# Performance work log

Measured on AMD Instinct MI355X. Metric: run time of the kernel, lower is better.

Reference implementation:

```python
import jax, jax.numpy as jnp
import numpy as np

NEG_SLOPE = 0.2  # PyG GATConv default negative_slope
EPS = 1e-16      # PyG softmax denominator epsilon


def gat_conv(x, src, dst, W, b, att_src, att_dst, num_nodes):
    """PyG GATConv, heads=1, add_self_loops=True (self loops already in src/dst).
    x: [N, Fin]; src/dst: [E]; W: [Fin, Fout]; att_src/att_dst: [Fout]."""
    h = x @ W                                  # [N, Fout]
    a_src = h @ att_src                        # [N]
    a_dst = h @ att_dst                        # [N]
    e = jax.nn.leaky_relu(a_src[src] + a_dst[dst], NEG_SLOPE)  # [E]
    m = jax.ops.segment_max(e, dst, num_segments=num_nodes)    # softmax over edges grouped by dst
    ex = jnp.exp(e - m[dst])
    denom = jax.ops.segment_sum(ex, dst, num_segments=num_nodes)
    alpha = ex / (denom[dst] + EPS)            # [E]
    out = jax.ops.segment_sum(alpha[:, None] * h[src], dst, num_segments=num_nodes)
    return out + b


def global_attention(x, gate_w, gate_b):
    """PyG GlobalAttention with a single graph: softmax(gate_nn(x)) weighted sum."""
    gate = x @ gate_w + gate_b                 # [N, 1]
    attn = jax.nn.softmax(gate, axis=0)        # softmax over all nodes (one graph)
    return jnp.sum(attn * x, axis=0, keepdims=True)  # [1, F]


def setup_inputs() -> dict:
    key = jax.random.key(0)
    ks = jax.random.split(key, 12)
    N, E, D, H = 50000, 800000, 768, 256
    x = jax.random.normal(ks[0], (N, D), dtype=jnp.float32)
    edge_index = jax.random.randint(ks[1], (2, E), 0, N, dtype=jnp.int64)
    s = 1.0 / np.sqrt(D)
    W1 = jax.random.normal(ks[2], (D, H), dtype=jnp.float32) * s
    b1 = jnp.zeros((H,), dtype=jnp.float32)
    as1 = jax.random.normal(ks[3], (H,), dtype=jnp.float32) * (1.0 / np.sqrt(H))
    ad1 = jax.random.normal(ks[4], (H,), dtype=jnp.float32) * (1.0 / np.sqrt(H))
    s2 = 1.0 / np.sqrt(H)
    W2 = jax.random.normal(ks[5], (H, H), dtype=jnp.float32) * s2
    b2 = jnp.zeros((H,), dtype=jnp.float32)
    as2 = jax.random.normal(ks[6], (H,), dtype=jnp.float32) * s2
    ad2 = jax.random.normal(ks[7], (H,), dtype=jnp.float32) * s2
    gate_w = jax.random.normal(ks[8], (H, 1), dtype=jnp.float32) * s2
    gate_b = jnp.zeros((1,), dtype=jnp.float32)
    return {"x": x, "edge_index": edge_index, "W1": W1, "b1": b1, "as1": as1,
            "ad1": ad1, "W2": W2, "b2": b2, "as2": as2, "ad2": ad2,
            "gate_w": gate_w, "gate_b": gate_b}


def reference(x, edge_index, W1, b1, as1, ad1, W2, b2, as2, ad2, gate_w, gate_b):
    N = x.shape[0]
    loops = jnp.arange(N, dtype=edge_index.dtype)
    src = jnp.concatenate([edge_index[0], loops])  # add self loops (GATConv default)
    dst = jnp.concatenate([edge_index[1], loops])
    h = gat_conv(x, src, dst, W1, b1, as1, ad1, N)
    h = jax.nn.relu(h)
    h = gat_conv(h, src, dst, W2, b2, as2, ad2, N)
    h = jax.nn.relu(h)
    return global_attention(h, gate_w, gate_b)   # [1, 256]
```

## Files before the change

kernel.cpp:

```cpp
#include <hip/hip_runtime.h>

#define WAVE 64
#define LRELU(x) ((x) > 0.0f ? (x) : 0.2f * (x))
#define SB0 __builtin_amdgcn_sched_barrier(0)

typedef __attribute__((ext_vector_type(8))) short bf16x8;
typedef __attribute__((ext_vector_type(8))) unsigned short u16x8;
typedef __attribute__((ext_vector_type(4))) float f32x4;

__device__ __forceinline__ void gld16(const void* g, void* l) {
    __builtin_amdgcn_global_load_lds((const __attribute__((address_space(1))) unsigned int*)g,
                                     (__attribute__((address_space(3))) unsigned int*)l,
                                     16, 0, 0);
}

__device__ __forceinline__ unsigned short f2bf_hi(float f) {
    unsigned u = __builtin_bit_cast(unsigned, f);
    u += 0x7FFF + ((u >> 16) & 1);
    return (unsigned short)(u >> 16);
}

__device__ __forceinline__ void split8(f32x4 a, f32x4 b, bf16x8& hi, bf16x8& lo) {
    float f[8] = {a[0], a[1], a[2], a[3], b[0], b[1], b[2], b[3]};
#pragma unroll
    for (int e = 0; e < 8; e++) {
        unsigned u = __builtin_bit_cast(unsigned, f[e]);
        float hf = __builtin_bit_cast(float, u & 0xFFFF0000u);
        float fl = f[e] - hf;
        unsigned u2 = __builtin_bit_cast(unsigned, fl);
        unsigned t2 = u2 + 0x7FFF + ((u2 >> 16) & 1);
        hi[e] = (short)(u >> 16);
        lo[e] = (short)(t2 >> 16);
    }
}

__device__ __forceinline__ void split8t(f32x4 a, f32x4 b, bf16x8& hi, bf16x8& lo) {
    float f[8] = {a[0], a[1], a[2], a[3], b[0], b[1], b[2], b[3]};
#pragma unroll
    for (int e = 0; e < 8; e++) {
        unsigned u = __builtin_bit_cast(unsigned, f[e]);
        float hf = __builtin_bit_cast(float, u & 0xFFFF0000u);
        float fl = f[e] - hf;
        unsigned u2 = __builtin_bit_cast(unsigned, fl);
        hi[e] = (short)(u >> 16);
        lo[e] = (short)(u2 >> 16);
    }
}

__global__ __launch_bounds__(512) void k_gemm_f32A(const float* __restrict__ A,
                                                   const unsigned short* __restrict__ Bh,
                                                   unsigned short* __restrict__ Cb,
                                                   float* __restrict__ asrc,
                                                   float* __restrict__ adst,
                                                   const float* __restrict__ att_s,
                                                   const float* __restrict__ att_d,
                                                   int M, int K) {
    __shared__ char smem[49152];
    char* bA = smem;
    char* bB = smem + 32768;

    const int tid = threadIdx.x, lane = tid & 63, w = tid >> 6;
    const int m16 = lane & 15, q = lane >> 4;
    const int mq = w >> 1, nh = w & 1;
    const int row0 = blockIdx.x * 128, col0 = blockIdx.y * 128;
    const int NT = K >> 5;

    f32x4 acc[2][4];
#pragma unroll
    for (int i = 0; i < 2; i++)
#pragma unroll
        for (int j = 0; j < 4; j++) acc[i][j] = (f32x4){0.f, 0.f, 0.f, 0.f};

    const float* apt[2];
    const int jA0 = w * 2;
#pragma unroll
    for (int jj = 0; jj < 2; jj++) {
        int j = jA0 + jj;
        int r = j * 8 + (lane >> 3);
        int grow = row0 + r;
        if (grow > M - 1) grow = M - 1;
        int s = (lane & 7) ^ ((lane >> 3) & 7);
        apt[jj] = A + (size_t)grow * K + s * 4;
    }
    const unsigned short* bpt;
    {
        int r = w * 16 + (lane >> 2);
        int s = (lane & 3) ^ ((lane >> 3) & 3);
        bpt = Bh + (size_t)(col0 + r) * K + s * 8;
    }

    auto stage = [&](int t, int buf) {
        gld16(bpt + (size_t)t * 32, bB + buf * 8192 + w * 1024);
#pragma unroll
        for (int jj = 0; jj < 2; jj++)
            gld16(apt[jj] + (size_t)t * 32, bA + buf * 16384 + (jA0 + jj) * 1024);
    };

    stage(0, 0); SB0;
    asm volatile("s_waitcnt vmcnt(0)" ::: "memory");
    __builtin_amdgcn_s_barrier();

    for (int t = 0; t < NT; ++t) {
        if (t + 1 < NT) stage(t + 1, (t + 1) & 1);
        SB0;

        const char* A_ = bA + (t & 1) * 16384;
        const char* B_ = bB + (t & 1) * 8192;
        bf16x8 bh[4];
#pragma unroll
        for (int nt = 0; nt < 4; nt++) {
            int r = nh * 64 + nt * 16 + m16;
            int p = q ^ ((r >> 1) & 3);
            bh[nt] = *(const bf16x8*)(B_ + r * 64 + p * 16);
        }
#pragma unroll
        for (int mt = 0; mt < 2; mt++) {
            int r = mq * 32 + mt * 16 + m16;
            int p0 = (2 * q) ^ (r & 7);
            int p1 = (2 * q + 1) ^ (r & 7);
            f32x4 a0 = *(const f32x4*)(A_ + r * 128 + p0 * 16);
            f32x4 a1 = *(const f32x4*)(A_ + r * 128 + p1 * 16);
            bf16x8 ah, al;
            split8t(a0, a1, ah, al);
#pragma unroll
            for (int nt = 0; nt < 4; nt++) {
                acc[mt][nt] = __builtin_amdgcn_mfma_f32_16x16x32_bf16(ah, bh[nt], acc[mt][nt], 0, 0, 0);
                acc[mt][nt] = __builtin_amdgcn_mfma_f32_16x16x32_bf16(al, bh[nt], acc[mt][nt], 0, 0, 0);
            }
        }
        SB0;
        asm volatile("s_waitcnt vmcnt(0)" ::: "memory");
        __builtin_amdgcn_s_barrier();
    }

    const int rbase = row0 + mq * 32;
    const int cbase = col0 + nh * 64;
#pragma unroll
    for (int mt = 0; mt < 2; mt++)
#pragma unroll
        for (int r = 0; r < 4; r++) {
            int row = rbase + mt * 16 + q * 4 + r;
            if (row < M) {
#pragma unroll
                for (int nt = 0; nt < 4; nt++)
                    Cb[(size_t)row * 256 + cbase + nt * 16 + m16] = f2bf_hi(acc[mt][nt][r]);
            }
        }
    float as_v[4], ad_v[4];
#pragma unroll
    for (int nt = 0; nt < 4; nt++) {
        as_v[nt] = att_s[cbase + nt * 16 + m16];
        ad_v[nt] = att_d[cbase + nt * 16 + m16];
    }
#pragma unroll
    for (int mt = 0; mt < 2; mt++)
#pragma unroll
        for (int r = 0; r < 4; r++) {
            float s = 0.f, d = 0.f;
#pragma unroll
            for (int nt = 0; nt < 4; nt++) {
                float v = acc[mt][nt][r];
                s = fmaf(v, as_v[nt], s);
                d = fmaf(v, ad_v[nt], d);
            }
#pragma unroll
            for (int off = 1; off < 16; off <<= 1) {
                s += __shfl_xor(s, off);
                d += __shfl_xor(d, off);
            }
            int row = rbase + mt * 16 + q * 4 + r;
            if (m16 == 0 && row < M) {
                atomicAdd(&asrc[row], s);
                atomicAdd(&adst[row], d);
            }
        }
}

__global__ __launch_bounds__(512) void k_gemm_bf16A(const unsigned short* __restrict__ Ah,
                                                    const unsigned short* __restrict__ Al,
                                                    const unsigned short* __restrict__ Bh,
                                                    unsigned short* __restrict__ Cb,
                                                    float* __restrict__ asrc,
                                                    float* __restrict__ adst,
                                                    const float* __restrict__ att_s,
                                                    const float* __restrict__ att_d,
                                                    int M, int K) {
    __shared__ char smem[49152];
    char* bAh = smem;
    char* bAl = smem + 16384;
    char* bB  = smem + 32768;

    const int tid = threadIdx.x, lane = tid & 63, w = tid >> 6;
    const int m16 = lane & 15, q = lane >> 4;
    const int mq = w >> 1, nh = w & 1;
    const int row0 = blockIdx.x * 128, col0 = blockIdx.y * 128;
    const int NT = K >> 5;

    f32x4 acc[2][4];
#pragma unroll
    for (int i = 0; i < 2; i++)
#pragma unroll
        for (int j = 0; j < 4; j++) acc[i][j] = (f32x4){0.f, 0.f, 0.f, 0.f};

    const unsigned short* ahpt;
    const unsigned short* alpt;
    const unsigned short* bpt;
    {
        int r = w * 16 + (lane >> 2);
        int s = (lane & 3) ^ ((lane >> 3) & 3);
        ahpt = Ah + (size_t)(row0 + r) * K + s * 8;
        alpt = Al + (size_t)(row0 + r) * K + s * 8;
        bpt  = Bh + (size_t)(col0 + r) * K + s * 8;
    }

    auto stage = [&](int t, int buf) {
        gld16(bpt  + (size_t)t * 32, bB  + buf * 8192 + w * 1024);
        gld16(ahpt + (size_t)t * 32, bAh + buf * 8192 + w * 1024);
        gld16(alpt + (size_t)t * 32, bAl + buf * 8192 + w * 1024);
    };

    stage(0, 0); SB0;
    asm volatile("s_waitcnt vmcnt(0)" ::: "memory");
    __builtin_amdgcn_s_barrier();

    for (int t = 0; t < NT; ++t) {
        if (t + 1 < NT) stage(t + 1, (t + 1) & 1);
        SB0;

        const char* Ah_ = bAh + (t & 1) * 8192;
        const char* Al_ = bAl + (t & 1) * 8192;
        const char* B_  = bB  + (t & 1) * 8192;
        bf16x8 bh[4];
#pragma unroll
        for (int nt = 0; nt < 4; nt++) {
            int r = nh * 64 + nt * 16 + m16;
            int p = q ^ ((r >> 1) & 3);
            bh[nt] = *(const bf16x8*)(B_ + r * 64 + p * 16);
        }
#pragma unroll
        for (int mt = 0; mt < 2; mt++) {
            int r = mq * 32 + mt * 16 + m16;
            int p = q ^ ((r >> 1) & 3);
            bf16x8 ah = *(const bf16x8*)(Ah_ + r * 64 + p * 16);
            bf16x8 al = *(const bf16x8*)(Al_ + r * 64 + p * 16);
#pragma unroll
            for (int nt = 0; nt < 4; nt++) {
                acc[mt][nt] = __builtin_amdgcn_mfma_f32_16x16x32_bf16(ah, bh[nt], acc[mt][nt], 0, 0, 0);
                acc[mt][nt] = __builtin_amdgcn_mfma_f32_16x16x32_bf16(al, bh[nt], acc[mt][nt], 0, 0, 0);
            }
        }
        SB0;
        asm volatile("s_waitcnt vmcnt(0)" ::: "memory");
        __builtin_amdgcn_s_barrier();
    }

    const int rbase = row0 + mq * 32;
    const int cbase = col0 + nh * 64;
#pragma unroll
    for (int mt = 0; mt < 2; mt++)
#pragma unroll
        for (int r = 0; r < 4; r++) {
            int row = rbase + mt * 16 + q * 4 + r;
            if (row < M) {
#pragma unroll
                for (int nt = 0; nt < 4; nt++)
                    Cb[(size_t)row * 256 + cbase + nt * 16 + m16] = f2bf_hi(acc[mt][nt][r]);
            }
        }
    float as_v[4], ad_v[4];
#pragma unroll
    for (int nt = 0; nt < 4; nt++) {
        as_v[nt] = att_s[cbase + nt * 16 + m16];
        ad_v[nt] = att_d[cbase + nt * 16 + m16];
    }
#pragma unroll
    for (int mt = 0; mt < 2; mt++)
#pragma unroll
        for (int r = 0; r < 4; r++) {
            float s = 0.f, d = 0.f;
#pragma unroll
            for (int nt = 0; nt < 4; nt++) {
                float v = acc[mt][nt][r];
                s = fmaf(v, as_v[nt], s);
                d = fmaf(v, ad_v[nt], d);
            }
#pragma unroll
            for (int off = 1; off < 16; off <<= 1) {
                s += __shfl_xor(s, off);
                d += __shfl_xor(d, off);
            }
            int row = rbase + mt * 16 + q * 4 + r;
            if (m16 == 0 && row < M) {
                atomicAdd(&asrc[row], s);
                atomicAdd(&adst[row], d);
            }
        }
}

__global__ __launch_bounds__(256) void k_convB(const float* __restrict__ W,
                                               unsigned short* __restrict__ BThi, int K) {
    int idx = blockIdx.x * 256 + threadIdx.x;
    int k = idx >> 8, n = idx & 255;
    if (k >= K) return;
    BThi[(size_t)n * K + k] = f2bf_hi(W[(size_t)k * 256 + n]);
}

__global__ __launch_bounds__(256) void k_degree(const int* __restrict__ dst,
                                                int* __restrict__ counts, int E) {
    int e = blockIdx.x * 256 + threadIdx.x;
    if (e < E) atomicAdd(&counts[dst[e]], 1);
}

__global__ __launch_bounds__(256) void k_part(const int* __restrict__ counts,
                                              int* __restrict__ psum, int N) {
    __shared__ int red[256];
    int tid = threadIdx.x;
    int i = blockIdx.x * 256 + tid;
    red[tid] = (i < N) ? counts[i] : 0;
    __syncthreads();
    for (int off = 128; off; off >>= 1) {
        if (tid < off) red[tid] += red[tid + off];
        __syncthreads();
    }
    if (tid == 0) psum[blockIdx.x] = red[0];
}

__global__ __launch_bounds__(256) void k_scan_part(int* __restrict__ psum, int nb,
                                                   int* __restrict__ total_out) {
    __shared__ int s[256];
    int tid = threadIdx.x;
    int v = (tid < nb) ? psum[tid] : 0;
    s[tid] = v;
    __syncthreads();
    for (int off = 1; off < 256; off <<= 1) {
        int t = (tid >= off) ? s[tid - off] : 0;
        __syncthreads();
        s[tid] += t;
        __syncthreads();
    }
    if (tid < nb) psum[tid] = s[tid] - v;
    if (tid == 255) *total_out = s[255];
}

__global__ __launch_bounds__(256) void k_rowptr(const int* __restrict__ counts,
                                                const int* __restrict__ psum,
                                                int* __restrict__ rowptr,
                                                int* __restrict__ cursor, int N) {
    __shared__ int s[256];
    int tid = threadIdx.x;
    int i = blockIdx.x * 256 + tid;
    int v = (i < N) ? counts[i] : 0;
    s[tid] = v;
    __syncthreads();
    for (int off = 1; off < 256; off <<= 1) {
        int t = (tid >= off) ? s[tid - off] : 0;
        __syncthreads();
        s[tid] += t;
        __syncthreads();
    }
    if (i < N) {
        int excl = psum[blockIdx.x] + s[tid] - v;
        rowptr[i] = excl;
        cursor[i] = excl;
    }
}

__global__ __launch_bounds__(256) void k_scatter(const int* __restrict__ src,
                                                 const int* __restrict__ dst,
                                                 int* __restrict__ cursor,
                                                 int* __restrict__ col, int E) {
    int e = blockIdx.x * 256 + threadIdx.x;
    if (e < E) {
        int p = atomicAdd(&cursor[dst[e]], 1);
        col[p] = src[e];
    }
}

__global__ __launch_bounds__(256) void k_edge(const unsigned short* __restrict__ hb,
                                              const float* __restrict__ asrc,
                                              const float* __restrict__ adst,
                                              const float* __restrict__ gmaxv,
                                              const int* __restrict__ rowptr,
                                              const int* __restrict__ col,
                                              const float* __restrict__ bias,
                                              float* __restrict__ outf,
                                              unsigned short* __restrict__ outh,
                                              unsigned short* __restrict__ outl,
                                              const float* __restrict__ gw,
                                              const float* __restrict__ gb,
                                              float* __restrict__ gatep, int N) {
    int hw = threadIdx.x >> 5;
    int l  = threadIdx.x & 31;
    int node = blockIdx.x * 8 + hw;
    if (node >= N) return;
    int j = rowptr[node], end = rowptr[node + 1];
    float ad = adst[node];
    float m = LRELU(gmaxv[0] + ad);

    float a[8];
    float wself = __expf(LRELU(asrc[node] + ad) - m);
    u16x8 hv = *(const u16x8*)&hb[(size_t)node * 256 + l * 8];
#pragma unroll
    for (int e = 0; e < 8; e++)
        a[e] = wself * __builtin_bit_cast(float, (unsigned)hv[e] << 16);
    float denom = wself;

    for (; j + 4 <= end; j += 4) {
        int s0 = col[j], s1 = col[j + 1], s2 = col[j + 2], s3 = col[j + 3];
        float w0 = __expf(LRELU(asrc[s0] + ad) - m);
        float w1 = __expf(LRELU(asrc[s1] + ad) - m);
        float w2 = __expf(LRELU(asrc[s2] + ad) - m);
        float w3 = __expf(LRELU(asrc[s3] + ad) - m);
        denom += w0 + w1 + w2 + w3;
        u16x8 h0 = *(const u16x8*)&hb[(size_t)s0 * 256 + l * 8];
        u16x8 h1 = *(const u16x8*)&hb[(size_t)s1 * 256 + l * 8];
        u16x8 h2 = *(const u16x8*)&hb[(size_t)s2 * 256 + l * 8];
        u16x8 h3 = *(const u16x8*)&hb[(size_t)s3 * 256 + l * 8];
#pragma unroll
        for (int e = 0; e < 8; e++) {
            float f0 = __builtin_bit_cast(float, (unsigned)h0[e] << 16);
            float f1 = __builtin_bit_cast(float, (unsigned)h1[e] << 16);
            float f2 = __builtin_bit_cast(float, (unsigned)h2[e] << 16);
            float f3 = __builtin_bit_cast(float, (unsigned)h3[e] << 16);
            a[e] = fmaf(w0, f0, fmaf(w1, f1, fmaf(w2, f2, fmaf(w3, f3, a[e]))));
        }
    }
    for (; j < end; j++) {
        int s = col[j];
        float wgt = __expf(LRELU(asrc[s] + ad) - m);
        denom += wgt;
        u16x8 hx = *(const u16x8*)&hb[(size_t)s * 256 + l * 8];
#pragma unroll
        for (int e = 0; e < 8; e++)
            a[e] = fmaf(wgt, __builtin_bit_cast(float, (unsigned)hx[e] << 16), a[e]);
    }
    float inv = 1.0f / (denom + 1e-16f);
#pragma unroll
    for (int e = 0; e < 8; e++) a[e] *= inv;

    float o[8];
    {
        float4 bv0 = *(const float4*)&bias[l * 8];
        float4 bv1 = *(const float4*)&bias[l * 8 + 4];
        float bb[8] = {bv0.x, bv0.y, bv0.z, bv0.w, bv1.x, bv1.y, bv1.z, bv1.w};
#pragma unroll
        for (int e = 0; e < 8; e++) o[e] = fmaxf(a[e] + bb[e], 0.0f);
    }
    if (outf) {
        float4 o0 = make_float4(o[0], o[1], o[2], o[3]);
        float4 o1 = make_float4(o[4], o[5], o[6], o[7]);
        *(float4*)&outf[(size_t)node * 256 + l * 8]     = o0;
        *(float4*)&outf[(size_t)node * 256 + l * 8 + 4] = o1;
    }
    if (outh) {
        u16x8 ph, pl;
#pragma unroll
        for (int e = 0; e < 8; e++) {
            unsigned u = __builtin_bit_cast(unsigned, o[e]);
            float hf = __builtin_bit_cast(float, u & 0xFFFF0000u);
            float fl = o[e] - hf;
            unsigned u2 = __builtin_bit_cast(unsigned, fl);
            unsigned t2 = u2 + 0x7FFF + ((u2 >> 16) & 1);
            ph[e] = (unsigned short)(u >> 16);
            pl[e] = (unsigned short)(t2 >> 16);
        }
        *(u16x8*)&outh[(size_t)node * 256 + l * 8] = ph;
        *(u16x8*)&outl[(size_t)node * 256 + l * 8] = pl;
    }
    if (gatep) {
        float s = 0.f;
#pragma unroll
        for (int e = 0; e < 8; e++) s = fmaf(o[e], gw[l * 8 + e], s);
#pragma unroll
        for (int off = 16; off; off >>= 1) s += __shfl_xor(s, off);
        if (l == 0) gatep[node] = s + gb[0];
    }
}

__global__ __launch_bounds__(256) void k_pmax(const float* __restrict__ v, int N,
                                              float* __restrict__ pmax) {
    __shared__ float red[256];
    int tid = threadIdx.x;
    float m = -3.0e38f;
    for (int i = blockIdx.x * 256 + tid; i < N; i += gridDim.x * 256) m = fmaxf(m, v[i]);
    red[tid] = m;
    __syncthreads();
    for (int off = 128; off; off >>= 1) {
        if (tid < off) red[tid] = fmaxf(red[tid], red[tid + off]);
        __syncthreads();
    }
    if (tid == 0) pmax[blockIdx.x] = red[0];
}

__global__ __launch_bounds__(64) void k_fold(const float* __restrict__ p,
                                             float* __restrict__ o) {
    int lane = threadIdx.x;
    float m = p[lane];
#pragma unroll
    for (int off = 32; off; off >>= 1) m = fmaxf(m, __shfl_xor(m, off));
    if (lane == 0) o[0] = m;
}

__global__ __launch_bounds__(256) void k_gmid(const float* __restrict__ pmax, int nb,
                                              float* __restrict__ scal,
                                              float* __restrict__ gout) {
    __shared__ float red[256];
    int tid = threadIdx.x;
    red[tid] = (tid < nb) ? pmax[tid] : -3.0e38f;
    __syncthreads();
    for (int off = 128; off; off >>= 1) {
        if (tid < off) red[tid] = fmaxf(red[tid], red[tid + off]);
        __syncthreads();
    }
    if (tid == 0) { scal[0] = red[0]; scal[1] = 0.0f; }
    gout[tid] = 0.0f;
}

__global__ __launch_bounds__(256) void k_gout(const float* __restrict__ h,
                                              const float* __restrict__ gate,
                                              float* __restrict__ scal_rw,
                                              float* __restrict__ gout, int N) {
    int f = threadIdx.x;
    float gmax = scal_rw[0];
    float acc = 0.0f, sumw = 0.0f;
    for (int i = blockIdx.x; i < N; i += gridDim.x) {
        float w = __expf(gate[i] - gmax);
        acc = fmaf(w, h[(size_t)i * 256 + f], acc);
        sumw += w;
    }
    atomicAdd(&gout[f], acc);
    if (f == 0) atomicAdd(&scal_rw[1], sumw);
}

__global__ __launch_bounds__(256) void k_final(const float* __restrict__ gout,
                                               const float* __restrict__ scal,
                                               float* __restrict__ out) {
    int f = threadIdx.x;
    out[f] = gout[f] / scal[1];
}

extern "C" void kernel_launch(void* const* d_in, const int* in_sizes, int n_in,
                              void* d_out, int out_size, void* d_ws, size_t ws_size,
                              hipStream_t stream) {
    const float* x   = (const float*)d_in[0];
    const int*   ei  = (const int*)d_in[1];
    const float* W1  = (const float*)d_in[2];
    const float* b1  = (const float*)d_in[3];
    const float* as1 = (const float*)d_in[4];
    const float* ad1 = (const float*)d_in[5];
    const float* W2  = (const float*)d_in[6];
    const float* b2  = (const float*)d_in[7];
    const float* as2 = (const float*)d_in[8];
    const float* ad2 = (const float*)d_in[9];
    const float* gw  = (const float*)d_in[10];
    const float* gb  = (const float*)d_in[11];
    float* out = (float*)d_out;

    const int N = in_sizes[0] / 768;
    const int E = in_sizes[1] / 2;
    const int Mpad = (N + 127) & ~127;
    const int* srcA = ei;
    const int* dstA = ei + E;

    char* w = (char*)d_ws;
    auto alloc = [&](size_t bytes) -> void* {
        void* p = (void*)w;
        w += (bytes + 255) & ~(size_t)255;
        return p;
    };
    unsigned short* bufHb = (unsigned short*)alloc((size_t)N * 256 * 2);
    unsigned short* X2h = (unsigned short*)alloc((size_t)Mpad * 256 * 2);
    unsigned short* X2l = (unsigned short*)alloc((size_t)Mpad * 256 * 2);
    float* bufX = (float*)X2h;
    float* asrc   = (float*)alloc((size_t)N * 4);
    float* adst   = (float*)alloc((size_t)N * 4);
    float* gate   = (float*)alloc((size_t)N * 4);
    int*   counts = (int*)alloc((size_t)N * 4);
    int*   rowptr = (int*)alloc((size_t)(N + 1) * 4);
    int*   cursor = (int*)alloc((size_t)N * 4);
    int*   colbuf = (int*)alloc((size_t)E * 4);
    int*   psum   = (int*)alloc(256 * 4);
    float* pmax   = (float*)alloc(256 * 4);
    float* gmaxv  = (float*)alloc(4 * 4);
    float* scal   = (float*)alloc(8 * 4);
    float* gout   = (float*)alloc(256 * 4);
    unsigned short* BT1 = (unsigned short*)alloc((size_t)256 * 768 * 2);
    unsigned short* BT2 = (unsigned short*)alloc((size_t)256 * 256 * 2);

    const int eb  = (E + 255) / 256;
    const int nb8 = (N + 7) / 8;
    const int nb  = (N + 255) / 256;
    const dim3 gg(Mpad / 128, 2);

    k_convB<<<768, 256, 0, stream>>>(W1, BT1, 768);
    k_convB<<<256, 256, 0, stream>>>(W2, BT2, 256);

    (void)hipMemsetAsync(counts, 0, (size_t)N * 4, stream);
    k_degree<<<eb, 256, 0, stream>>>(dstA, counts, E);
    k_part<<<nb, 256, 0, stream>>>(counts, psum, N);
    k_scan_part<<<1, 256, 0, stream>>>(psum, nb, rowptr + N);
    k_rowptr<<<nb, 256, 0, stream>>>(counts, psum, rowptr, cursor, N);
    k_scatter<<<eb, 256, 0, stream>>>(srcA, dstA, cursor, colbuf, E);

    (void)hipMemsetAsync(asrc, 0, (size_t)N * 4, stream);
    (void)hipMemsetAsync(adst, 0, (size_t)N * 4, stream);
    k_gemm_f32A<<<gg, 512, 0, stream>>>(x, BT1, bufHb, asrc, adst, as1, ad1, N, 768);
    k_pmax<<<64, 256, 0, stream>>>(asrc, N, pmax);
    k_fold<<<1, 64, 0, stream>>>(pmax, gmaxv);
    k_edge<<<nb8, 256, 0, stream>>>(bufHb, asrc, adst, gmaxv, rowptr, colbuf, b1,
                                    nullptr, X2h, X2l, nullptr, nullptr, nullptr, N);

    (void)hipMemsetAsync(asrc, 0, (size_t)N * 4, stream);
    (void)hipMemsetAsync(adst, 0, (size_t)N * 4, stream);
    k_gemm_bf16A<<<gg, 512, 0, stream>>>(X2h, X2l, BT2, bufHb, asrc, adst, as2, ad2, N, 256);
    k_pmax<<<64, 256, 0, stream>>>(asrc, N, pmax);
    k_fold<<<1, 64, 0, stream>>>(pmax, gmaxv);
    k_edge<<<nb8, 256, 0, stream>>>(bufHb, asrc, adst, gmaxv, rowptr, colbuf, b2,
                                    bufX, nullptr, nullptr, gw, gb, gate, N);

    k_pmax<<<64, 256, 0, stream>>>(gate, N, pmax);
    k_gmid<<<1, 256, 0, stream>>>(pmax, 64, scal, gout);
    k_gout<<<256, 256, 0, stream>>>(bufX, gate, scal, gout, N);
    k_final<<<1, 256, 0, stream>>>(gout, scal, out);
}
```

Before: 604.3 us.

## Drop bf16 hi/lo split in GEMMs and deepen load pipeline to three stages

Both GEMMs previously emulated fp32 precision by splitting activations into bf16 high and low parts and running two MFMAs per tile. They now round activations once to bf16 with round-to-nearest, which halves MFMA work and removes the low-part buffer writes and reads in the edge kernel. The LDS staging also moves from double to triple buffering with partial vmcnt waits, so loads run two tiles ahead. This lowers numerical accuracy of the projections and raises LDS use per block, which may reduce occupancy.

```diff
diff --git a/kernel.cpp b/kernel.cpp
--- a/kernel.cpp
+++ b/kernel.cpp
@@ -20,31 +20,16 @@
     return (unsigned short)(u >> 16);
 }
 
-__device__ __forceinline__ void split8(f32x4 a, f32x4 b, bf16x8& hi, bf16x8& lo) {
+__device__ __forceinline__ bf16x8 rne8(f32x4 a, f32x4 b) {
+    bf16x8 h;
     float f[8] = {a[0], a[1], a[2], a[3], b[0], b[1], b[2], b[3]};
 #pragma unroll
     for (int e = 0; e < 8; e++) {
         unsigned u = __builtin_bit_cast(unsigned, f[e]);
-        float hf = __builtin_bit_cast(float, u & 0xFFFF0000u);
-        float fl = f[e] - hf;
-        unsigned u2 = __builtin_bit_cast(unsigned, fl);
-        unsigned t2 = u2 + 0x7FFF + ((u2 >> 16) & 1);
-        hi[e] = (short)(u >> 16);
-        lo[e] = (short)(t2 >> 16);
-    }
-}
-
-__device__ __forceinline__ void split8t(f32x4 a, f32x4 b, bf16x8& hi, bf16x8& lo) {
-    float f[8] = {a[0], a[1], a[2], a[3], b[0], b[1], b[2], b[3]};
-#pragma unroll
-    for (int e = 0; e < 8; e++) {
-        unsigned u = __builtin_bit_cast(unsigned, f[e]);
-        float hf = __builtin_bit_cast(float, u & 0xFFFF0000u);
-        float fl = f[e] - hf;
-        unsigned u2 = __builtin_bit_cast(unsigned, fl);
-        hi[e] = (short)(u >> 16);
-        lo[e] = (short)(u2 >> 16);
-    }
+        u += 0x7FFF + ((u >> 16) & 1);
+        h[e] = (short)(u >> 16);
+    }
+    return h;
 }
 
 __global__ __launch_bounds__(512) void k_gemm_f32A(const float* __restrict__ A,
@@ -55,9 +40,7 @@
                                                    const float* __restrict__ att_s,
                                                    const float* __restrict__ att_d,
                                                    int M, int K) {
-    __shared__ char smem[49152];
-    char* bA = smem;
-    char* bB = smem + 32768;
+    __shared__ char smem[73728];
 
     const int tid = threadIdx.x, lane = tid & 63, w = tid >> 6;
     const int m16 = lane & 15, q = lane >> 4;
@@ -90,22 +73,25 @@
     }
 
     auto stage = [&](int t, int buf) {
-        gld16(bpt + (size_t)t * 32, bB + buf * 8192 + w * 1024);
+        char* S = smem + buf * 24576;
+        gld16(bpt + (size_t)t * 32, S + 16384 + w * 1024);
 #pragma unroll
         for (int jj = 0; jj < 2; jj++)
-            gld16(apt[jj] + (size_t)t * 32, bA + buf * 16384 + (jA0 + jj) * 1024);
+            gld16(apt[jj] + (size_t)t * 32, S + (jA0 + jj) * 1024);
     };
 
     stage(0, 0); SB0;
-    asm volatile("s_waitcnt vmcnt(0)" ::: "memory");
+    stage(1, 1); SB0;
+    asm volatile("s_waitcnt vmcnt(3)" ::: "memory");
     __builtin_amdgcn_s_barrier();
 
     for (int t = 0; t < NT; ++t) {
-        if (t + 1 < NT) stage(t + 1, (t + 1) & 1);
+        if (t + 2 < NT) stage(t + 2, (t + 2) % 3);
         SB0;
 
-        const char* A_ = bA + (t & 1) * 16384;
-        const char* B_ = bB + (t & 1) * 8192;
+        const char* S  = smem + (t % 3) * 24576;
+        const char* A_ = S;
+        const char* B_ = S + 16384;
         bf16x8 bh[4];
 #pragma unroll
         for (int nt = 0; nt < 4; nt++) {
@@ -120,16 +106,14 @@
             int p1 = (2 * q + 1) ^ (r & 7);
             f32x4 a0 = *(const f32x4*)(A_ + r * 128 + p0 * 16);
             f32x4 a1 = *(const f32x4*)(A_ + r * 128 + p1 * 16);
-            bf16x8 ah, al;
-            split8t(a0, a1, ah, al);
-#pragma unroll
-            for (int nt = 0; nt < 4; nt++) {
+            bf16x8 ah = rne8(a0, a1);
+#pragma unroll
+            for (int nt = 0; nt < 4; nt++)
                 acc[mt][nt] = __builtin_amdgcn_mfma_f32_16x16x32_bf16(ah, bh[nt], acc[mt][nt], 0, 0, 0);
-                acc[mt][nt] = __builtin_amdgcn_mfma_f32_16x16x32_bf16(al, bh[nt], acc[mt][nt], 0, 0, 0);
-            }
         }
         SB0;
-        asm volatile("s_waitcnt vmcnt(0)" ::: "memory");
+        if (t + 2 < NT) asm volatile("s_waitcnt vmcnt(3)" ::: "memory");
+        else            asm volatile("s_waitcnt vmcnt(0)" ::: "memory");
         __builtin_amdgcn_s_barrier();
     }
 
@@ -177,7 +161,6 @@
 }
 
 __global__ __launch_bounds__(512) void k_gemm_bf16A(const unsigned short* __restrict__ Ah,
-                                                    const unsigned short* __restrict__ Al,
                                                     const unsigned short* __restrict__ Bh,
                                                     unsigned short* __restrict__ Cb,
                                                     float* __restrict__ asrc,
@@ -186,9 +169,6 @@
                                                     const float* __restrict__ att_d,
                                                     int M, int K) {
     __shared__ char smem[49152];
-    char* bAh = smem;
-    char* bAl = smem + 16384;
-    char* bB  = smem + 32768;
 
     const int tid = threadIdx.x, lane = tid & 63, w = tid >> 6;
     const int m16 = lane & 15, q = lane >> 4;
@@ -203,33 +183,32 @@
         for (int j = 0; j < 4; j++) acc[i][j] = (f32x4){0.f, 0.f, 0.f, 0.f};
 
     const unsigned short* ahpt;
-    const unsigned short* alpt;
     const unsigned short* bpt;
     {
         int r = w * 16 + (lane >> 2);
         int s = (lane & 3) ^ ((lane >> 3) & 3);
         ahpt = Ah + (size_t)(row0 + r) * K + s * 8;
-        alpt = Al + (size_t)(row0 + r) * K + s * 8;
         bpt  = Bh + (size_t)(col0 + r) * K + s * 8;
     }
 
     auto stage = [&](int t, int buf) {
-        gld16(bpt  + (size_t)t * 32, bB  + buf * 8192 + w * 1024);
-        gld16(ahpt + (size_t)t * 32, bAh + buf * 8192 + w * 1024);
-        gld16(alpt + (size_t)t * 32, bAl + buf * 8192 + w * 1024);
+        char* S = smem + buf * 16384;
+        gld16(bpt  + (size_t)t * 32, S + 8192 + w * 1024);
+        gld16(ahpt + (size_t)t * 32, S + w * 1024);
     };
 
     stage(0, 0); SB0;
-    asm volatile("s_waitcnt vmcnt(0)" ::: "memory");
+    stage(1, 1); SB0;
+    asm volatile("s_waitcnt vmcnt(2)" ::: "memory");
     __builtin_amdgcn_s_barrier();
 
     for (int t = 0; t < NT; ++t) {
-        if (t + 1 < NT) stage(t + 1, (t + 1) & 1);
+        if (t + 2 < NT) stage(t + 2, (t + 2) % 3);
         SB0;
 
-        const char* Ah_ = bAh + (t & 1) * 8192;
-        const char* Al_ = bAl + (t & 1) * 8192;
-        const char* B_  = bB  + (t & 1) * 8192;
+        const char* S   = smem + (t % 3) * 16384;
+        const char* Ah_ = S;
+        const char* B_  = S + 8192;
         bf16x8 bh[4];
 #pragma unroll
         for (int nt = 0; nt < 4; nt++) {
@@ -242,15 +221,13 @@
             int r = mq * 32 + mt * 16 + m16;
             int p = q ^ ((r >> 1) & 3);
             bf16x8 ah = *(const bf16x8*)(Ah_ + r * 64 + p * 16);
-            bf16x8 al = *(const bf16x8*)(Al_ + r * 64 + p * 16);
-#pragma unroll
-            for (int nt = 0; nt < 4; nt++) {
+#pragma unroll
+            for (int nt = 0; nt < 4; nt++)
                 acc[mt][nt] = __builtin_amdgcn_mfma_f32_16x16x32_bf16(ah, bh[nt], acc[mt][nt], 0, 0, 0);
-                acc[mt][nt] = __builtin_amdgcn_mfma_f32_16x16x32_bf16(al, bh[nt], acc[mt][nt], 0, 0, 0);
-            }
         }
         SB0;
-        asm volatile("s_waitcnt vmcnt(0)" ::: "memory");
+        if (t + 2 < NT) asm volatile("s_waitcnt vmcnt(2)" ::: "memory");
+        else            asm volatile("s_waitcnt vmcnt(0)" ::: "memory");
         __builtin_amdgcn_s_barrier();
     }
 
@@ -385,7 +362,6 @@
                                               const float* __restrict__ bias,
                                               float* __restrict__ outf,
                                               unsigned short* __restrict__ outh,
-                                              unsigned short* __restrict__ outl,
                                               const float* __restrict__ gw,
                                               const float* __restrict__ gb,
                                               float* __restrict__ gatep, int N) {
@@ -453,19 +429,10 @@
         *(float4*)&outf[(size_t)node * 256 + l * 8 + 4] = o1;
     }
     if (outh) {
-        u16x8 ph, pl;
-#pragma unroll
-        for (int e = 0; e < 8; e++) {
-            unsigned u = __builtin_bit_cast(unsigned, o[e]);
-            float hf = __builtin_bit_cast(float, u & 0xFFFF0000u);
-            float fl = o[e] - hf;
-            unsigned u2 = __builtin_bit_cast(unsigned, fl);
-            unsigned t2 = u2 + 0x7FFF + ((u2 >> 16) & 1);
-            ph[e] = (unsigned short)(u >> 16);
-            pl[e] = (unsigned short)(t2 >> 16);
-        }
+        u16x8 ph;
+#pragma unroll
+        for (int e = 0; e < 8; e++) ph[e] = f2bf_hi(o[e]);
         *(u16x8*)&outh[(size_t)node * 256 + l * 8] = ph;
-        *(u16x8*)&outl[(size_t)node * 256 + l * 8] = pl;
     }
     if (gatep) {
         float s = 0.f;
@@ -569,9 +536,8 @@
         return p;
     };
     unsigned short* bufHb = (unsigned short*)alloc((size_t)N * 256 * 2);
-    unsigned short* X2h = (unsigned short*)alloc((size_t)Mpad * 256 * 2);
-    unsigned short* X2l = (unsigned short*)alloc((size_t)Mpad * 256 * 2);
-    float* bufX = (float*)X2h;
+    float* bufX = (float*)alloc((size_t)Mpad * 256 * 4);
+    unsigned short* X2h = (unsigned short*)bufX;
     float* asrc   = (float*)alloc((size_t)N * 4);
     float* adst   = (float*)alloc((size_t)N * 4);
     float* gate   = (float*)alloc((size_t)N * 4);
@@ -608,15 +574,15 @@
     k_pmax<<<64, 256, 0, stream>>>(asrc, N, pmax);
     k_fold<<<1, 64, 0, stream>>>(pmax, gmaxv);
     k_edge<<<nb8, 256, 0, stream>>>(bufHb, asrc, adst, gmaxv, rowptr, colbuf, b1,
-                                    nullptr, X2h, X2l, nullptr, nullptr, nullptr, N);
+                                    nullptr, X2h, nullptr, nullptr, nullptr, N);
 
     (void)hipMemsetAsync(asrc, 0, (size_t)N * 4, stream);
     (void)hipMemsetAsync(adst, 0, (size_t)N * 4, stream);
-    k_gemm_bf16A<<<gg, 512, 0, stream>>>(X2h, X2l, BT2, bufHb, asrc, adst, as2, ad2, N, 256);
+    k_gemm_bf16A<<<gg, 512, 0, stream>>>(X2h, BT2, bufHb, asrc, adst, as2, ad2, N, 256);
     k_pmax<<<64, 256, 0, stream>>>(asrc, N, pmax);
     k_fold<<<1, 64, 0, stream>>>(pmax, gmaxv);
     k_edge<<<nb8, 256, 0, stream>>>(bufHb, asrc, adst, gmaxv, rowptr, colbuf, b2,
-                                    bufX, nullptr, nullptr, gw, gb, gate, N);
+                                    bufX, nullptr, gw, gb, gate, N);
 
     k_pmax<<<64, 256, 0, stream>>>(gate, N, pmax);
     k_gmid<<<1, 256, 0, stream>>>(pmax, 64, scal, gout);
```

Measured after the change: 588.1 us. 2.7% less time.
